# Kernel optimization log

Hardware: AMD Instinct MI355X
Metric: run time of the kernel (lower is better)

The kernel has to match this reference:

```python
import jax, jax.numpy as jnp
import numpy as np

N, E = 50000, 800000
IN, HID, HEADS, OUT = 128, 64, 2, 32
SLOPE = 0.2  # PyG leaky_relu default


def gat_conv(x, edge_index, edge_attr, W, att_src, att_dst, W_edge, att_edge, bias,
             heads, out_ch, concat):
    n = x.shape[0]
    src, dst = edge_index[0], edge_index[1]
    # add_self_loops with fill_value='mean': self-loop attr = mean of incoming edge_attr
    ones = jnp.ones((src.shape[0],), x.dtype)
    deg = jax.ops.segment_sum(ones, dst, num_segments=n)
    loop_attr = jax.ops.segment_sum(edge_attr, dst, num_segments=n) / jnp.maximum(deg, 1.0)[:, None]
    ar = jnp.arange(n)
    src = jnp.concatenate([src, ar])
    dst = jnp.concatenate([dst, ar])
    ea = jnp.concatenate([edge_attr, loop_attr], axis=0)  # [E+N, 1]
    # linear projections
    h = (x @ W).reshape(n, heads, out_ch)                      # [N,H,C]
    a_src = jnp.sum(h * att_src, axis=-1)                      # [N,H]
    a_dst = jnp.sum(h * att_dst, axis=-1)                      # [N,H]
    e_emb = (ea @ W_edge).reshape(-1, heads, out_ch)           # [E+N,H,C]
    a_edge = jnp.sum(e_emb * att_edge, axis=-1)                # [E+N,H]
    alpha = jax.nn.leaky_relu(a_src[src] + a_dst[dst] + a_edge, SLOPE)
    # segment softmax over destination nodes
    amax = jax.ops.segment_max(alpha, dst, num_segments=n)
    amax = jnp.where(jnp.isfinite(amax), amax, 0.0)
    ex = jnp.exp(alpha - amax[dst])
    denom = jax.ops.segment_sum(ex, dst, num_segments=n)
    coef = ex / (denom[dst] + 1e-16)                           # [E+N,H]
    out = jax.ops.segment_sum(h[src] * coef[:, :, None], dst, num_segments=n)  # [N,H,C]
    out = out.reshape(n, heads * out_ch) if concat else out.mean(axis=1)
    return out + bias


def setup_inputs() -> dict:
    key = jax.random.key(0)
    ks = jax.random.split(key, 16)
    g = lambda k, shape, fan: (jax.random.normal(k, shape, jnp.float32) / np.float32(np.sqrt(fan)))
    x = jax.random.normal(ks[0], (N, IN), jnp.float32)
    edge_index = jax.random.randint(ks[1], (2, E), 0, N)
    edge_weight = jax.random.uniform(ks[2], (E, 1), jnp.float32)
    return dict(
        x=x, edge_index=edge_index, edge_weight=edge_weight,
        W1=g(ks[3], (IN, HEADS * HID), IN),
        att_src1=g(ks[4], (1, HEADS, HID), HID),
        att_dst1=g(ks[5], (1, HEADS, HID), HID),
        We1=g(ks[6], (1, HEADS * HID), 1),
        att_edge1=g(ks[7], (1, HEADS, HID), HID),
        b1=jnp.zeros((HEADS * HID,), jnp.float32),
        W2=g(ks[8], (HEADS * HID, OUT), HEADS * HID),
        att_src2=g(ks[9], (1, 1, OUT), OUT),
        att_dst2=g(ks[10], (1, 1, OUT), OUT),
        We2=g(ks[11], (1, OUT), 1),
        att_edge2=g(ks[12], (1, 1, OUT), OUT),
        b2=jnp.zeros((OUT,), jnp.float32),
    )


def reference(x, edge_index, edge_weight, W1, att_src1, att_dst1, We1, att_edge1, b1,
              W2, att_src2, att_dst2, We2, att_edge2, b2):
    h = gat_conv(x, edge_index, edge_weight, W1, att_src1, att_dst1, We1, att_edge1, b1,
                 HEADS, HID, True)
    h = jax.nn.elu(h)
    out = gat_conv(h, edge_index, edge_weight, W2, att_src2, att_dst2, We2, att_edge2, b2,
                   1, OUT, False)
    return out
```

## Files before the change

kernel.cpp:

```cpp
#include <hip/hip_runtime.h>
#include <hip/hip_bf16.h>
#include <hip/hip_fp16.h>
#include <cstddef>

#define NN 50000
#define EE 800000
#define SB  196
#define EB  3125
#define GB  782
#define ZB  1563

typedef _Float16 half4v __attribute__((ext_vector_type(4)));
typedef _Float16 half8v __attribute__((ext_vector_type(8)));
typedef _Float16 h2v    __attribute__((ext_vector_type(2)));
typedef float    f32x4  __attribute__((ext_vector_type(4)));

__global__ void init_k(unsigned* __restrict__ dreg,
                       const float* __restrict__ We1, const float* __restrict__ attE1,
                       const float* __restrict__ We2, const float* __restrict__ attE2,
                       float* __restrict__ cE) {
    int t = threadIdx.x;
    if (blockIdx.x == ZB) {
        __shared__ float smc[128];
        if (t < 128) smc[t] = We1[t] * attE1[t];
        __syncthreads();
        for (int off = 32; off; off >>= 1) {
            if (t < 128 && (t & 63) < off) smc[t] += smc[t + off];
            __syncthreads();
        }
        if (t == 0)  cE[0] = smc[0];
        if (t == 64) cE[1] = smc[64];
        __syncthreads();
        if (t < 32) smc[t] = We2[t] * attE2[t];
        __syncthreads();
        for (int off = 16; off; off >>= 1) {
            if (t < off) smc[t] += smc[t + off];
            __syncthreads();
        }
        if (t == 0) cE[2] = smc[0];
        return;
    }
    int i = blockIdx.x * 256 + t;
    if (i < 8 * NN) dreg[i] = 0u;
}

__global__ void hist_k(const int* __restrict__ ei, unsigned* __restrict__ dreg,
                       int* __restrict__ rank) {
    int e = blockIdx.x * 256 + threadIdx.x;
    if (e >= EE) return;
    int dst = ei[EE + e];
    int rep = blockIdx.x & 7;
    rank[e] = (int)atomicAdd(&dreg[rep * NN + dst], 1u);
}

__global__ void combine_k(const unsigned* __restrict__ dreg, int* __restrict__ deg,
                          unsigned short* __restrict__ repbase, int* __restrict__ bsum) {
    __shared__ int sm[256];
    int t = threadIdx.x, n = blockIdx.x * 256 + t;
    int d = 0;
    if (n < NN) {
        unsigned base = 0;
        #pragma unroll
        for (int r = 0; r < 8; r++) {
            unsigned c = dreg[r * NN + n];
            repbase[r * NN + n] = (unsigned short)base;
            base += c;
        }
        d = (int)base;
        deg[n] = d;
    }
    sm[t] = d;
    __syncthreads();
    for (int off = 128; off; off >>= 1) {
        if (t < off) sm[t] += sm[t + off];
        __syncthreads();
    }
    if (!t) bsum[blockIdx.x] = sm[0];
}

__global__ void scan_final_k(const int* __restrict__ deg, const int* __restrict__ bsum,
                             int* __restrict__ rowptr) {
    __shared__ int sm[256];
    __shared__ int boff_s;
    int t = threadIdx.x, b = blockIdx.x, i = b * 256 + t;
    int v0 = (t < b) ? bsum[t] : 0;
    sm[t] = v0;
    __syncthreads();
    for (int off = 128; off; off >>= 1) {
        if (t < off) sm[t] += sm[t + off];
        __syncthreads();
    }
    if (!t) boff_s = sm[0];
    __syncthreads();
    int v = (i < NN) ? deg[i] : 0;
    sm[t] = v;
    __syncthreads();
    for (int off = 1; off < 256; off <<= 1) {
        int a = (t >= off) ? sm[t - off] : 0;
        __syncthreads();
        sm[t] += a;
        __syncthreads();
    }
    if (i < NN) rowptr[i] = boff_s + sm[t] - v;
    if (i == NN - 1) rowptr[NN] = boff_s + sm[t];
}

__global__ void scatter_k(const int* __restrict__ ei, const float* __restrict__ ew,
                          const int* __restrict__ rowptr,
                          const unsigned short* __restrict__ repbase,
                          const int* __restrict__ rank, int2* __restrict__ csr) {
    int e = blockIdx.x * 256 + threadIdx.x;
    if (e >= EE) return;
    int src = ei[e];
    int dst = ei[EE + e];
    int rep = blockIdx.x & 7;
    int pos = rowptr[dst] + (int)repbase[rep * NN + dst] + rank[e];
    csr[pos] = make_int2(src, __float_as_int(ew[e]));
}

__global__ __launch_bounds__(256) void gemm1_k(const float* __restrict__ x,
                                               const float* __restrict__ W,
                                               const float* __restrict__ attS,
                                               const float* __restrict__ attD,
                                               __half* __restrict__ h1,
                                               float* __restrict__ asrc,
                                               float* __restrict__ adst) {
    __shared__ __align__(16) _Float16 xs[64 * 136];
    int rowbase = blockIdx.x * 64;
    int t = threadIdx.x;
    int wid = t >> 6, lane = t & 63;
    #pragma unroll
    for (int i = 0; i < 8; i++) {
        int idx = t + i * 256;
        int r = idx >> 5;
        int c4 = idx & 31;
        float4 v = make_float4(0.f, 0.f, 0.f, 0.f);
        if (rowbase + r < NN) v = ((const float4*)x)[(size_t)(rowbase + r) * 32 + c4];
        half4v hv = { (_Float16)v.x, (_Float16)v.y, (_Float16)v.z, (_Float16)v.w };
        *(half4v*)&xs[r * 136 + c4 * 4] = hv;
    }
    half8v bf[2][4];
    #pragma unroll
    for (int nt = 0; nt < 2; nt++)
        #pragma unroll
        for (int kk = 0; kk < 4; kk++) {
            int kb = kk * 32 + ((lane >> 4) << 3);
            int c = (wid << 5) + (nt << 4) + (lane & 15);
            half8v f;
            #pragma unroll
            for (int j = 0; j < 8; j++) f[j] = (_Float16)W[(kb + j) * 128 + c];
            bf[nt][kk] = f;
        }
    __syncthreads();
    int ar = lane & 15;
    int ak = (lane >> 4) << 3;
    f32x4 acc[4][2] = {};
    #pragma unroll
    for (int kk = 0; kk < 4; kk++) {
        half8v a[4];
        #pragma unroll
        for (int mt = 0; mt < 4; mt++)
            a[mt] = *(const half8v*)&xs[(mt * 16 + ar) * 136 + kk * 32 + ak];
        #pragma unroll
        for (int mt = 0; mt < 4; mt++)
            #pragma unroll
            for (int nt = 0; nt < 2; nt++)
                acc[mt][nt] = __builtin_amdgcn_mfma_f32_16x16x32_f16(
                    a[mt], bf[nt][kk], acc[mt][nt], 0, 0, 0);
    }
    __syncthreads();
    int drb = (lane >> 4) << 2;
    int dc = (wid << 5) + (lane & 15);
    #pragma unroll
    for (int mt = 0; mt < 4; mt++)
        #pragma unroll
        for (int nt = 0; nt < 2; nt++)
            #pragma unroll
            for (int r = 0; r < 4; r++)
                xs[(mt * 16 + drb + r) * 136 + dc + nt * 16] = (_Float16)acc[mt][nt][r];
    __syncthreads();
    int row = t >> 2;
    int cg = t & 3;
    int grow = rowbase + row;
    float sv = 0.f, dv = 0.f;
    #pragma unroll
    for (int k = 0; k < 4; k++) {
        int c0 = cg * 32 + k * 8;
        half8v hv = *(const half8v*)&xs[row * 136 + c0];
        if (grow < NN) *(half8v*)((_Float16*)h1 + (size_t)grow * 128 + c0) = hv;
        #pragma unroll
        for (int j = 0; j < 8; j++) {
            float f = (float)hv[j];
            sv += f * attS[c0 + j];
            dv += f * attD[c0 + j];
        }
    }
    sv += __shfl_xor(sv, 1);
    dv += __shfl_xor(dv, 1);
    if ((cg & 1) == 0 && grow < NN) {
        asrc[grow * 2 + (cg >> 1)] = sv;
        adst[grow * 2 + (cg >> 1)] = dv;
    }
}

__global__ __launch_bounds__(256) void gemm2_k(const __half* __restrict__ z1,
                                               const float* __restrict__ W,
                                               const float* __restrict__ attS,
                                               const float* __restrict__ attD,
                                               __half* __restrict__ h2,
                                               float* __restrict__ asrc,
                                               float* __restrict__ adst) {
    __shared__ __align__(16) _Float16 xs[64 * 136];
    int rowbase = blockIdx.x * 64;
    int t = threadIdx.x;
    int wid = t >> 6, lane = t & 63;
    #pragma unroll
    for (int i = 0; i < 4; i++) {
        int idx = t + i * 256;
        int r = idx >> 4;
        int c16 = idx & 15;
        uint4 v = make_uint4(0, 0, 0, 0);
        if (rowbase + r < NN) v = ((const uint4*)z1)[(size_t)(rowbase + r) * 16 + c16];
        *(uint4*)&xs[r * 136 + c16 * 8] = v;
    }
    half8v bf[2][4];
    #pragma unroll
    for (int nt = 0; nt < 2; nt++)
        #pragma unroll
        for (int kk = 0; kk < 4; kk++) {
            int kb = kk * 32 + ((lane >> 4) << 3);
            int c = (nt << 4) + (lane & 15);
            half8v f;
            #pragma unroll
            for (int j = 0; j < 8; j++) f[j] = (_Float16)W[(kb + j) * 32 + c];
            bf[nt][kk] = f;
        }
    __syncthreads();
    int ar = lane & 15;
    int ak = (lane >> 4) << 3;
    f32x4 acc[2] = {};
    #pragma unroll
    for (int kk = 0; kk < 4; kk++) {
        half8v a = *(const half8v*)&xs[(wid * 16 + ar) * 136 + kk * 32 + ak];
        #pragma unroll
        for (int nt = 0; nt < 2; nt++)
            acc[nt] = __builtin_amdgcn_mfma_f32_16x16x32_f16(a, bf[nt][kk], acc[nt], 0, 0, 0);
    }
    __syncthreads();
    int drb = (lane >> 4) << 2;
    #pragma unroll
    for (int nt = 0; nt < 2; nt++)
        #pragma unroll
        for (int r = 0; r < 4; r++)
            xs[(wid * 16 + drb + r) * 40 + (nt << 4) + (lane & 15)] = (_Float16)acc[nt][r];
    __syncthreads();
    int row = t >> 2;
    int c8 = (t & 3) * 8;
    int grow = rowbase + row;
    half8v hv = *(const half8v*)&xs[row * 40 + c8];
    if (grow < NN) *(half8v*)((_Float16*)h2 + (size_t)grow * 32 + c8) = hv;
    float sv = 0.f, dv = 0.f;
    #pragma unroll
    for (int j = 0; j < 8; j++) {
        float f = (float)hv[j];
        sv += f * attS[c8 + j];
        dv += f * attD[c8 + j];
    }
    sv += __shfl_xor(sv, 1);
    dv += __shfl_xor(dv, 1);
    sv += __shfl_xor(sv, 2);
    dv += __shfl_xor(dv, 2);
    if ((t & 3) == 0 && grow < NN) { asrc[grow] = sv; adst[grow] = dv; }
}

__global__ __launch_bounds__(256) void agg1_k(const int* __restrict__ rowptr,
                       const int2* __restrict__ csr,
                       const __half* __restrict__ h1, const float* __restrict__ asrc,
                       const float* __restrict__ adst, const float* __restrict__ cE,
                       const float* __restrict__ b1, __half* __restrict__ z1) {
    __shared__ int    ssrc[4][128];
    __shared__ float2 sxx[4][128];
    __shared__ int2   spk[4][136];
    int wid = threadIdx.x >> 6;
    int n = (blockIdx.x * blockDim.x + threadIdx.x) >> 6;
    int lane = threadIdx.x & 63;
    if (n >= NN) return;
    int start = rowptr[n];
    int degn = rowptr[n + 1] - start;
    int total = degn + 1;
    float c0 = cE[0], c1 = cE[1];
    float ad0 = adst[n * 2], ad1 = adst[n * 2 + 1];
    float s0 = 0.f, s1 = 0.f, sumw = 0.f;
    for (int i = lane; i < degn; i += 64) {
        int2 sw = csr[start + i];
        int src = sw.x;
        float w = __int_as_float(sw.y);
        sumw += w;
        float2 as = *(const float2*)&asrc[src * 2];
        float e0 = as.x + ad0 + w * c0; e0 = e0 > 0.f ? e0 : 0.2f * e0;
        float e1 = as.y + ad1 + w * c1; e1 = e1 > 0.f ? e1 : 0.2f * e1;
        float x0 = __expf(e0), x1 = __expf(e1);
        s0 += x0; s1 += x1;
        if (i < 128) { ssrc[wid][i] = src; sxx[wid][i] = make_float2(x0, x1); }
    }
    for (int off = 32; off; off >>= 1) {
        s0 += __shfl_xor(s0, off);
        s1 += __shfl_xor(s1, off);
        sumw += __shfl_xor(sumw, off);
    }
    float la = sumw / fmaxf((float)degn, 1.0f);
    float2 asn = *(const float2*)&asrc[n * 2];
    float el0 = asn.x + ad0 + la * c0; el0 = el0 > 0.f ? el0 : 0.2f * el0;
    float el1 = asn.y + ad1 + la * c1; el1 = el1 > 0.f ? el1 : 0.2f * el1;
    float xl0 = __expf(el0), xl1 = __expf(el1);
    s0 += xl0; s1 += xl1;
    if (degn < 128 && lane == (degn & 63)) {
        ssrc[wid][degn] = n;
        sxx[wid][degn] = make_float2(xl0, xl1);
    }
    float inv0 = 1.0f / (s0 + 1e-16f), inv1 = 1.0f / (s1 + 1e-16f);
    int nst = min(total, 128);
    int nst8 = (nst + 7) & ~7;
    for (int i = lane; i < nst8; i += 64) {
        int2 pk;
        if (i < nst) {
            float2 xv = sxx[wid][i];
            __half2 hh = __floats2half2_rn(xv.x * inv0, xv.y * inv1);
            pk = make_int2(ssrc[wid][i], *(int*)&hh);
        } else pk = make_int2(n, 0);
        spk[wid][i] = pk;
    }
    int hsel = lane >> 5;
    unsigned psel = hsel ? 0x03020302u : 0x01000100u;
    unsigned loff = (unsigned)lane * 4u;
    const char* h1b_ = (const char*)h1;
    float acc0 = 0.f, acc1 = 0.f;
    for (int j = 0; j < nst8; j += 8) {
        h2v pa = {}, pb = {};
        #pragma unroll
        for (int u = 0; u < 8; u++) {
            int2 st = spk[wid][j + u];
            unsigned cs = __builtin_amdgcn_perm(0u, (unsigned)st.y, psel);
            unsigned hb = *(const unsigned*)(h1b_ + (((unsigned)st.x << 8) + loff));
            h2v c; __builtin_memcpy(&c, &cs, 4);
            h2v h; __builtin_memcpy(&h, &hb, 4);
            if (u & 1) pb = c * h + pb;
            else       pa = c * h + pa;
        }
        acc0 += (float)pa.x + (float)pb.x;
        acc1 += (float)pa.y + (float)pb.y;
    }
    for (int base = 128; base < total; base += 64) {
        int i = base + lane;
        float cc0 = 0.f, cc1 = 0.f; int src = n;
        if (i < total) {
            float w;
            if (i < degn) { int2 sw = csr[start + i]; src = sw.x; w = __int_as_float(sw.y); }
            else          { w = la; }
            float e0 = asrc[src * 2]     + ad0 + w * c0; e0 = e0 > 0.f ? e0 : 0.2f * e0;
            float e1 = asrc[src * 2 + 1] + ad1 + w * c1; e1 = e1 > 0.f ? e1 : 0.2f * e1;
            cc0 = __expf(e0) * inv0;
            cc1 = __expf(e1) * inv1;
        }
        int cnt = min(64, total - base);
        for (int jj = 0; jj < cnt; jj++) {
            int   s2 = __shfl(src, jj);
            float k0 = __shfl(cc0, jj);
            float k1 = __shfl(cc1, jj);
            float coef = hsel ? k1 : k0;
            float2 f = __half22float2(*(const __half2*)&h1[(size_t)s2 * 128 + 2 * lane]);
            acc0 += coef * f.x;
            acc1 += coef * f.y;
        }
    }
    float o0 = acc0 + b1[2 * lane];
    float o1 = acc1 + b1[2 * lane + 1];
    o0 = o0 > 0.f ? o0 : expm1f(o0);
    o1 = o1 > 0.f ? o1 : expm1f(o1);
    __half2 oz = __floats2half2_rn(o0, o1);
    *(__half2*)&z1[(size_t)n * 128 + 2 * lane] = oz;
}

__global__ __launch_bounds__(256) void agg2_k(const int* __restrict__ rowptr,
                       const int2* __restrict__ csr,
                       const __half* __restrict__ hh2, const float* __restrict__ asrc,
                       const float* __restrict__ adst, const float* __restrict__ cE,
                       const float* __restrict__ b2, float* __restrict__ out) {
    __shared__ float2 sxx[4][128];
    __shared__ int    ssrc[4][128];
    __shared__ int2   spk[4][136];
    int wid = threadIdx.x >> 6;
    int n = (blockIdx.x * blockDim.x + threadIdx.x) >> 6;
    int lane = threadIdx.x & 63;
    if (n >= NN) return;
    int start = rowptr[n];
    int degn = rowptr[n + 1] - start;
    int total = degn + 1;
    float c2 = cE[2];
    float aD = adst[n];
    float s = 0.f, sumw = 0.f;
    for (int i = lane; i < degn; i += 64) {
        int2 sw = csr[start + i];
        int src = sw.x;
        float w = __int_as_float(sw.y);
        sumw += w;
        float e = asrc[src] + aD + w * c2;
        e = e > 0.f ? e : 0.2f * e;
        float x = __expf(e);
        s += x;
        if (i < 128) { ssrc[wid][i] = src; sxx[wid][i] = make_float2(x, 0.f); }
    }
    for (int off = 32; off; off >>= 1) {
        s += __shfl_xor(s, off);
        sumw += __shfl_xor(sumw, off);
    }
    float la = sumw / fmaxf((float)degn, 1.0f);
    float el = asrc[n] + aD + la * c2; el = el > 0.f ? el : 0.2f * el;
    float xl = __expf(el);
    s += xl;
    if (degn < 128 && lane == (degn & 63)) {
        ssrc[wid][degn] = n;
        sxx[wid][degn] = make_float2(xl, 0.f);
    }
    float inv = 1.0f / (s + 1e-16f);
    int nst = min(total, 128);
    int nst8 = (nst + 7) & ~7;
    for (int i = lane; i < nst8; i += 64) {
        int2 pk;
        if (i < nst) {
            float cn = sxx[wid][i].x * inv;
            __half2 hc = __floats2half2_rn(cn, cn);
            pk = make_int2(ssrc[wid][i], *(int*)&hc);
        } else pk = make_int2(n, 0);
        spk[wid][i] = pk;
    }
    int g  = lane >> 4;
    int cp = lane & 15;
    const char* h2b_ = (const char*)hh2;
    unsigned coff = (unsigned)cp * 4u;
    float fa0 = 0.f, fa1 = 0.f;
    h2v pa = {}, pb = {};
    int fold = 0;
    for (int j = 0; j < nst8; j += 8) {
        int2 st0 = spk[wid][j + g];
        int2 st1 = spk[wid][j + 4 + g];
        unsigned hb0 = *(const unsigned*)(h2b_ + (((unsigned)st0.x << 6) + coff));
        unsigned hb1 = *(const unsigned*)(h2b_ + (((unsigned)st1.x << 6) + coff));
        h2v c0v; __builtin_memcpy(&c0v, &st0.y, 4);
        h2v c1v; __builtin_memcpy(&c1v, &st1.y, 4);
        h2v h0; __builtin_memcpy(&h0, &hb0, 4);
        h2v h1v; __builtin_memcpy(&h1v, &hb1, 4);
        pa = c0v * h0 + pa;
        pb = c1v * h1v + pb;
        if (++fold == 4) {
            fa0 += (float)pa.x + (float)pb.x;
            fa1 += (float)pa.y + (float)pb.y;
            pa = {}; pb = {};
            fold = 0;
        }
    }
    fa0 += (float)pa.x + (float)pb.x;
    fa1 += (float)pa.y + (float)pb.y;
    for (int i = 128; i < total; i++) {
        int src; float w;
        if (i < degn) { int2 sw = csr[start + i]; src = sw.x; w = __int_as_float(sw.y); }
        else          { src = n;                  w = la; }
        float e = asrc[src] + aD + w * c2;
        e = e > 0.f ? e : 0.2f * e;
        float cc = __expf(e) * inv;
        if (g == 0) {
            unsigned hb = *(const unsigned*)(h2b_ + (((unsigned)src << 6) + coff));
            h2v h; __builtin_memcpy(&h, &hb, 4);
            fa0 += cc * (float)h.x;
            fa1 += cc * (float)h.y;
        }
    }
    fa0 += __shfl_xor(fa0, 16); fa1 += __shfl_xor(fa1, 16);
    fa0 += __shfl_xor(fa0, 32); fa1 += __shfl_xor(fa1, 32);
    if (lane < 16) {
        float2 o = make_float2(fa0 + b2[2 * cp], fa1 + b2[2 * cp + 1]);
        *(float2*)&out[(size_t)n * 32 + 2 * cp] = o;
    }
}

extern "C" void kernel_launch(void* const* d_in, const int* in_sizes, int n_in,
                              void* d_out, int out_size, void* d_ws, size_t ws_size,
                              hipStream_t stream) {
    const float* x     = (const float*)d_in[0];
    const int*   ei    = (const int*)d_in[1];
    const float* ew    = (const float*)d_in[2];
    const float* W1    = (const float*)d_in[3];
    const float* attS1 = (const float*)d_in[4];
    const float* attD1 = (const float*)d_in[5];
    const float* We1   = (const float*)d_in[6];
    const float* attE1 = (const float*)d_in[7];
    const float* b1    = (const float*)d_in[8];
    const float* W2    = (const float*)d_in[9];
    const float* attS2 = (const float*)d_in[10];
    const float* attD2 = (const float*)d_in[11];
    const float* We2   = (const float*)d_in[12];
    const float* attE2 = (const float*)d_in[13];
    const float* b2    = (const float*)d_in[14];

    char* ws = (char*)d_ws;
    size_t off = 0;
    auto alloc = [&](size_t bytes) -> void* {
        void* p = ws + off;
        off = (off + bytes + 255) & ~(size_t)255;
        return p;
    };
    unsigned*       dreg    = (unsigned*)alloc((size_t)NN * 8 * 4);
    unsigned short* repbase = (unsigned short*)alloc((size_t)NN * 8 * 2);
    int*    rank    = (int*)alloc((size_t)EE * 4);
    int*    deg     = (int*)alloc((size_t)NN * 4);
    int*    rowptr  = (int*)alloc((size_t)(NN + 1) * 4);
    int2*   csr     = (int2*)alloc((size_t)EE * 8);
    __half* h1b     = (__half*)alloc((size_t)NN * 128 * 2);
    __half* z1      = (__half*)alloc((size_t)NN * 128 * 2);
    __half* h2b     = (__half*)alloc((size_t)NN * 32 * 2);
    float*  asrc1   = (float*)alloc((size_t)NN * 2 * 4);
    float*  adst1   = (float*)alloc((size_t)NN * 2 * 4);
    float*  asrc2   = (float*)alloc((size_t)NN * 4);
    float*  adst2   = (float*)alloc((size_t)NN * 4);
    float*  cE      = (float*)alloc(4 * 4);
    int*    bsum    = (int*)alloc(256 * 4);

    const int NWB = (NN * 64 + 255) / 256;

    init_k<<<ZB + 1, 256, 0, stream>>>(dreg, We1, attE1, We2, attE2, cE);
    hist_k<<<EB, 256, 0, stream>>>(ei, dreg, rank);
    combine_k<<<SB, 256, 0, stream>>>(dreg, deg, repbase, bsum);
    scan_final_k<<<SB, 256, 0, stream>>>(deg, bsum, rowptr);
    scatter_k<<<EB, 256, 0, stream>>>(ei, ew, rowptr, repbase, rank, csr);

    gemm1_k<<<GB, 256, 0, stream>>>(x, W1, attS1, attD1, h1b, asrc1, adst1);
    agg1_k<<<NWB, 256, 0, stream>>>(rowptr, csr, h1b, asrc1, adst1, cE, b1, z1);

    gemm2_k<<<GB, 256, 0, stream>>>(z1, W2, attS2, attD2, h2b, asrc2, adst2);
    agg2_k<<<NWB, 256, 0, stream>>>(rowptr, csr, h2b, asrc2, adst2, cE, b2, (float*)d_out);
}
```

Before: 147.5 us.

## Fuse edge histogram with layer-1 GEMM in one launch and precompute per-replica row bases

The degree histogram and the layer-1 projection GEMM now run in one kernel. Three of every four blocks do grid-strided atomic histogram work and the fourth does a GEMM tile, so the atomic-bound and compute-bound work can overlap on the GPU. The scan kernel now also writes a combined rowptr+repbase array (rowbase8), so the scatter does one gather instead of two. The replica index now comes from the edge index rather than the block id. The cost is an extra NN*8 int buffer and one fewer launch, with the overlap depending on how the block scheduler interleaves the two roles.

```diff
diff --git a/kernel.cpp b/kernel.cpp
--- a/kernel.cpp
+++ b/kernel.cpp
@@ -6,9 +6,10 @@
 #define NN 50000
 #define EE 800000
 #define SB  196
-#define EB  3125
 #define GB  782
 #define ZB  1563
+#define FT  4096
+#define HBK 3072
 
 typedef _Float16 half4v __attribute__((ext_vector_type(4)));
 typedef _Float16 half8v __attribute__((ext_vector_type(8)));
@@ -44,90 +45,26 @@
     if (i < 8 * NN) dreg[i] = 0u;
 }
 
-__global__ void hist_k(const int* __restrict__ ei, unsigned* __restrict__ dreg,
-                       int* __restrict__ rank) {
-    int e = blockIdx.x * 256 + threadIdx.x;
-    if (e >= EE) return;
-    int dst = ei[EE + e];
-    int rep = blockIdx.x & 7;
-    rank[e] = (int)atomicAdd(&dreg[rep * NN + dst], 1u);
-}
-
-__global__ void combine_k(const unsigned* __restrict__ dreg, int* __restrict__ deg,
-                          unsigned short* __restrict__ repbase, int* __restrict__ bsum) {
-    __shared__ int sm[256];
-    int t = threadIdx.x, n = blockIdx.x * 256 + t;
-    int d = 0;
-    if (n < NN) {
-        unsigned base = 0;
-        #pragma unroll
-        for (int r = 0; r < 8; r++) {
-            unsigned c = dreg[r * NN + n];
-            repbase[r * NN + n] = (unsigned short)base;
-            base += c;
-        }
-        d = (int)base;
-        deg[n] = d;
-    }
-    sm[t] = d;
-    __syncthreads();
-    for (int off = 128; off; off >>= 1) {
-        if (t < off) sm[t] += sm[t + off];
-        __syncthreads();
-    }
-    if (!t) bsum[blockIdx.x] = sm[0];
-}
-
-__global__ void scan_final_k(const int* __restrict__ deg, const int* __restrict__ bsum,
-                             int* __restrict__ rowptr) {
-    __shared__ int sm[256];
-    __shared__ int boff_s;
-    int t = threadIdx.x, b = blockIdx.x, i = b * 256 + t;
-    int v0 = (t < b) ? bsum[t] : 0;
-    sm[t] = v0;
-    __syncthreads();
-    for (int off = 128; off; off >>= 1) {
-        if (t < off) sm[t] += sm[t + off];
-        __syncthreads();
-    }
-    if (!t) boff_s = sm[0];
-    __syncthreads();
-    int v = (i < NN) ? deg[i] : 0;
-    sm[t] = v;
-    __syncthreads();
-    for (int off = 1; off < 256; off <<= 1) {
-        int a = (t >= off) ? sm[t - off] : 0;
-        __syncthreads();
-        sm[t] += a;
-        __syncthreads();
-    }
-    if (i < NN) rowptr[i] = boff_s + sm[t] - v;
-    if (i == NN - 1) rowptr[NN] = boff_s + sm[t];
-}
-
-__global__ void scatter_k(const int* __restrict__ ei, const float* __restrict__ ew,
-                          const int* __restrict__ rowptr,
-                          const unsigned short* __restrict__ repbase,
-                          const int* __restrict__ rank, int2* __restrict__ csr) {
-    int e = blockIdx.x * 256 + threadIdx.x;
-    if (e >= EE) return;
-    int src = ei[e];
-    int dst = ei[EE + e];
-    int rep = blockIdx.x & 7;
-    int pos = rowptr[dst] + (int)repbase[rep * NN + dst] + rank[e];
-    csr[pos] = make_int2(src, __float_as_int(ew[e]));
-}
-
-__global__ __launch_bounds__(256) void gemm1_k(const float* __restrict__ x,
-                                               const float* __restrict__ W,
-                                               const float* __restrict__ attS,
-                                               const float* __restrict__ attD,
-                                               __half* __restrict__ h1,
-                                               float* __restrict__ asrc,
-                                               float* __restrict__ adst) {
+__global__ __launch_bounds__(256) void histgemm_k(
+        const int* __restrict__ ei, unsigned* __restrict__ dreg, int* __restrict__ rank,
+        const float* __restrict__ x, const float* __restrict__ W,
+        const float* __restrict__ attS, const float* __restrict__ attD,
+        __half* __restrict__ h1, float* __restrict__ asrc, float* __restrict__ adst) {
     __shared__ __align__(16) _Float16 xs[64 * 136];
-    int rowbase = blockIdx.x * 64;
     int t = threadIdx.x;
+    int b = blockIdx.x;
+    if ((b & 3) != 3) {
+        int hb = (b >> 2) * 3 + (b & 3);
+        for (int e = hb * 256 + t; e < EE; e += HBK * 256) {
+            int dst = ei[EE + e];
+            int rep = (e >> 8) & 7;
+            rank[e] = (int)atomicAdd(&dreg[rep * NN + dst], 1u);
+        }
+        return;
+    }
+    int tile = b >> 2;
+    if (tile >= GB) return;
+    int rowbase = tile * 64;
     int wid = t >> 6, lane = t & 63;
     #pragma unroll
     for (int i = 0; i < 8; i++) {
@@ -201,6 +138,77 @@
         asrc[grow * 2 + (cg >> 1)] = sv;
         adst[grow * 2 + (cg >> 1)] = dv;
     }
+}
+
+__global__ void combine_k(const unsigned* __restrict__ dreg, int* __restrict__ deg,
+                          unsigned short* __restrict__ repbase, int* __restrict__ bsum) {
+    __shared__ int sm[256];
+    int t = threadIdx.x, n = blockIdx.x * 256 + t;
+    int d = 0;
+    if (n < NN) {
+        unsigned base = 0;
+        #pragma unroll
+        for (int r = 0; r < 8; r++) {
+            unsigned c = dreg[r * NN + n];
+            repbase[r * NN + n] = (unsigned short)base;
+            base += c;
+        }
+        d = (int)base;
+        deg[n] = d;
+    }
+    sm[t] = d;
+    __syncthreads();
+    for (int off = 128; off; off >>= 1) {
+        if (t < off) sm[t] += sm[t + off];
+        __syncthreads();
+    }
+    if (!t) bsum[blockIdx.x] = sm[0];
+}
+
+__global__ void scan_final_k(const int* __restrict__ deg, const int* __restrict__ bsum,
+                             const unsigned short* __restrict__ repbase,
+                             int* __restrict__ rowptr, int* __restrict__ rowbase8) {
+    __shared__ int sm[256];
+    __shared__ int boff_s;
+    int t = threadIdx.x, b = blockIdx.x, i = b * 256 + t;
+    int v0 = (t < b) ? bsum[t] : 0;
+    sm[t] = v0;
+    __syncthreads();
+    for (int off = 128; off; off >>= 1) {
+        if (t < off) sm[t] += sm[t + off];
+        __syncthreads();
+    }
+    if (!t) boff_s = sm[0];
+    __syncthreads();
+    int v = (i < NN) ? deg[i] : 0;
+    sm[t] = v;
+    __syncthreads();
+    for (int off = 1; off < 256; off <<= 1) {
+        int a = (t >= off) ? sm[t - off] : 0;
+        __syncthreads();
+        sm[t] += a;
+        __syncthreads();
+    }
+    if (i < NN) {
+        int rp = boff_s + sm[t] - v;
+        rowptr[i] = rp;
+        #pragma unroll
+        for (int r = 0; r < 8; r++)
+            rowbase8[r * NN + i] = rp + (int)repbase[r * NN + i];
+    }
+    if (i == NN - 1) rowptr[NN] = boff_s + sm[t];
+}
+
+__global__ void scatter_k(const int* __restrict__ ei, const float* __restrict__ ew,
+                          const int* __restrict__ rowbase8,
+                          const int* __restrict__ rank, int2* __restrict__ csr) {
+    int e = blockIdx.x * 256 + threadIdx.x;
+    if (e >= EE) return;
+    int src = ei[e];
+    int dst = ei[EE + e];
+    int rep = (e >> 8) & 7;
+    int pos = rowbase8[rep * NN + dst] + rank[e];
+    csr[pos] = make_int2(src, __float_as_int(ew[e]));
 }
 
 __global__ __launch_bounds__(256) void gemm2_k(const __half* __restrict__ z1,
@@ -509,8 +517,9 @@
         off = (off + bytes + 255) & ~(size_t)255;
         return p;
     };
-    unsigned*       dreg    = (unsigned*)alloc((size_t)NN * 8 * 4);
-    unsigned short* repbase = (unsigned short*)alloc((size_t)NN * 8 * 2);
+    unsigned*       dreg     = (unsigned*)alloc((size_t)NN * 8 * 4);
+    unsigned short* repbase  = (unsigned short*)alloc((size_t)NN * 8 * 2);
+    int*            rowbase8 = (int*)alloc((size_t)NN * 8 * 4);
     int*    rank    = (int*)alloc((size_t)EE * 4);
     int*    deg     = (int*)alloc((size_t)NN * 4);
     int*    rowptr  = (int*)alloc((size_t)(NN + 1) * 4);
@@ -525,17 +534,17 @@
     float*  cE      = (float*)alloc(4 * 4);
     int*    bsum    = (int*)alloc(256 * 4);
 
+    const int EB  = (EE + 255) / 256;
     const int NWB = (NN * 64 + 255) / 256;
 
     init_k<<<ZB + 1, 256, 0, stream>>>(dreg, We1, attE1, We2, attE2, cE);
-    hist_k<<<EB, 256, 0, stream>>>(ei, dreg, rank);
+    histgemm_k<<<FT, 256, 0, stream>>>(ei, dreg, rank, x, W1, attS1, attD1,
+                                       h1b, asrc1, adst1);
     combine_k<<<SB, 256, 0, stream>>>(dreg, deg, repbase, bsum);
-    scan_final_k<<<SB, 256, 0, stream>>>(deg, bsum, rowptr);
-    scatter_k<<<EB, 256, 0, stream>>>(ei, ew, rowptr, repbase, rank, csr);
-
-    gemm1_k<<<GB, 256, 0, stream>>>(x, W1, attS1, attD1, h1b, asrc1, adst1);
+    scan_final_k<<<SB, 256, 0, stream>>>(deg, bsum, repbase, rowptr, rowbase8);
+    scatter_k<<<EB, 256, 0, stream>>>(ei, ew, rowbase8, rank, csr);
+
     agg1_k<<<NWB, 256, 0, stream>>>(rowptr, csr, h1b, asrc1, adst1, cE, b1, z1);
-
     gemm2_k<<<GB, 256, 0, stream>>>(z1, W2, attS2, attD2, h2b, asrc2, adst2);
     agg2_k<<<NWB, 256, 0, stream>>>(rowptr, csr, h2b, asrc2, adst2, cE, b2, (float*)d_out);
 }
```

After: 156.4 us. 6.0% more time.
